# Kernel optimization log

Hardware: AMD Instinct MI355X
Metric: run time of the kernel (lower is better)

## Reference

```python
import jax, jax.numpy as jnp
import numpy as np

B, N, H = 4, 1024, 64

def setup_inputs() -> dict:
    key = jax.random.key(0)
    k1, k2, k3 = jax.random.split(key, 3)
    x = jax.random.normal(k1, (B, N, H), dtype=jnp.float32)
    # nn.Linear(2H, H): weight [H, 2H], bias [H]
    s1 = 1.0 / np.sqrt(2 * H)
    W1 = jax.random.uniform(k2, (H, 2 * H), minval=-s1, maxval=s1, dtype=jnp.float32)
    b1 = jnp.zeros((H,), dtype=jnp.float32)
    # nn.Linear(H, 1): weight [1, H], bias [1]
    s2 = 1.0 / np.sqrt(H)
    W2 = jax.random.uniform(k3, (1, H), minval=-s2, maxval=s2, dtype=jnp.float32)
    b2 = jnp.zeros((1,), dtype=jnp.float32)
    return {"x": x, "W1": W1, "b1": b1, "W2": W2, "b2": b2}

def reference(x, W1, b1, W2, b2):
    # cat([x_i, x_j]) @ W1.T == x_i @ W1a.T + x_j @ W1b.T  (decomposed; same math)
    W1a, W1b = W1[:, :x.shape[-1]], W1[:, x.shape[-1]:]
    hi = jnp.einsum('bid,hd->bih', x, W1a)            # [B,N,H]
    hj = jnp.einsum('bjd,hd->bjh', x, W1b)            # [B,N,H]
    h = jax.nn.relu(hi[:, :, None, :] + hj[:, None, :, :] + b1)  # [B,N,N,H]
    logits = jnp.einsum('bijh,h->bij', h, W2[0]) + b2[0]          # [B,N,N]
    attn = jax.nn.softmax(logits, axis=-1)
    updated = jnp.einsum('bij,bjd->bid', attn, x)     # [B,N,H]
    return updated, attn
```

## Files before the change

### kernel.cpp

```cpp
#include <hip/hip_runtime.h>

#define ATTN_OFF 262144

#define WS_HIP  0
#define WS_HJP  131072
#define WS_L16  262144
#define WS_SMAX 2359296
#define WS_SSUM 2424832
#define WS_PART 2490368

typedef float4 f4;
typedef _Float16 h2v __attribute__((ext_vector_type(2)));

union F4H { f4 f; h2v h[4]; };
union F2H { float2 f; h2v h[2]; };

__device__ __forceinline__ f4 ld4(const float* p) { return *reinterpret_cast<const f4*>(p); }
__device__ __forceinline__ void st4(float* p, f4 v) { *reinterpret_cast<f4*>(p) = v; }
__device__ __forceinline__ float fdot2f(h2v a, h2v b, float c) {
    return __builtin_amdgcn_fdot2(a, b, c, false);
}
__device__ __forceinline__ h2v pack2(float a, float b) {
    h2v r; r.x = (_Float16)a; r.y = (_Float16)b; return r;
}

__global__ __launch_bounds__(256, 4)
void ka_proj(const float* __restrict__ x, const float* __restrict__ W1,
             const float* __restrict__ b1,
             h2v* __restrict__ hiP, h2v* __restrict__ hjP) {
    __shared__ float xT[64 * 68];
    __shared__ float w1T[64 * 68];
    const int t  = threadIdx.x;
    const int i0 = blockIdx.x * 64;
    const int b  = blockIdx.y;
    const int z  = blockIdx.z;
    const int lo = t & 15;
    const int dq = t >> 4;
#pragma unroll
    for (int p = 0; p < 4; ++p) {
        const int il = p * 16 + lo;
        f4 v = ld4(&x[(size_t)(b * 1024 + i0 + il) * 64 + dq * 4]);
        xT[(dq * 4 + 0) * 68 + il] = v.x;
        xT[(dq * 4 + 1) * 68 + il] = v.y;
        xT[(dq * 4 + 2) * 68 + il] = v.z;
        xT[(dq * 4 + 3) * 68 + il] = v.w;
        f4 w = ld4(&W1[(size_t)il * 128 + z * 64 + dq * 4]);
        w1T[(dq * 4 + 0) * 68 + il] = w.x;
        w1T[(dq * 4 + 1) * 68 + il] = w.y;
        w1T[(dq * 4 + 2) * 68 + il] = w.z;
        w1T[(dq * 4 + 3) * 68 + il] = w.w;
    }
    __syncthreads();
    const int tx = t & 15;
    const int ty = t >> 4;
    float acc[4][4];
    if (z == 0) {
        f4 bv = ld4(&b1[tx * 4]);
        float ba[4] = {bv.x, bv.y, bv.z, bv.w};
#pragma unroll
        for (int ii = 0; ii < 4; ++ii)
#pragma unroll
            for (int cc = 0; cc < 4; ++cc) acc[ii][cc] = ba[cc];
    } else {
#pragma unroll
        for (int ii = 0; ii < 4; ++ii)
#pragma unroll
            for (int cc = 0; cc < 4; ++cc) acc[ii][cc] = 0.f;
    }
#pragma unroll 8
    for (int d = 0; d < 64; ++d) {
        f4 xv = ld4(&xT[d * 68 + ty * 4]);
        f4 wv = ld4(&w1T[d * 68 + tx * 4]);
        float xa[4] = {xv.x, xv.y, xv.z, xv.w};
        float wa[4] = {wv.x, wv.y, wv.z, wv.w};
#pragma unroll
        for (int ii = 0; ii < 4; ++ii)
#pragma unroll
            for (int cc = 0; cc < 4; ++cc)
                acc[ii][cc] = fmaf(xa[ii], wa[cc], acc[ii][cc]);
    }
    h2v* outp = z ? hjP : hiP;
#pragma unroll
    for (int p = 0; p < 2; ++p) {
        F4H u;
#pragma unroll
        for (int ii = 0; ii < 4; ++ii)
            u.h[ii] = pack2(acc[ii][p * 2 + 0], acc[ii][p * 2 + 1]);
        st4((float*)&outp[(size_t)(b * 32 + tx * 2 + p) * 1024 + i0 + ty * 4], u.f);
    }
}

__global__ __launch_bounds__(256, 4)
void kb_logits(const h2v* __restrict__ hiP, const h2v* __restrict__ hjP,
               const float* __restrict__ W2, _Float16* __restrict__ l16,
               float* __restrict__ smax, float* __restrict__ ssum) {
    __shared__ __align__(16) h2v s_hi[32 * 128];
    __shared__ __align__(16) h2v s_hj[32 * 64];
    __shared__ h2v s_w2[32];
    const int t  = threadIdx.x;
    const int jT = blockIdx.x;
    const int iT = blockIdx.y;
    const int b  = blockIdx.z;
#pragma unroll
    for (int p = 0; p < 4; ++p) {
        const int idx = p * 256 + t;
        const int hp  = idx >> 5;
        const int c4  = (idx & 31) * 4;
        st4((float*)&s_hi[hp * 128 + c4],
            ld4((const float*)&hiP[(size_t)(b * 32 + hp) * 1024 + iT * 128 + c4]));
    }
#pragma unroll
    for (int p = 0; p < 2; ++p) {
        const int idx = p * 256 + t;
        const int hp  = idx >> 4;
        const int c4  = (idx & 15) * 4;
        st4((float*)&s_hj[hp * 64 + c4],
            ld4((const float*)&hjP[(size_t)(b * 32 + hp) * 1024 + jT * 64 + c4]));
    }
    if (t < 16) {
        f4 w = ld4(&W2[t * 4]);
        s_w2[t * 2]     = pack2(w.x, w.y);
        s_w2[t * 2 + 1] = pack2(w.z, w.w);
    }
    __syncthreads();
    const int tx = t & 15;
    const int ty = t >> 4;
    float acc[8][4];
#pragma unroll
    for (int ii = 0; ii < 8; ++ii)
#pragma unroll
        for (int jj = 0; jj < 4; ++jj) acc[ii][jj] = 0.f;
    const h2v z2 = (h2v)0;
#pragma unroll 4
    for (int hp = 0; hp < 32; ++hp) {
        F4H a0, a1, bb;
        a0.f = ld4((const float*)&s_hi[hp * 128 + ty * 8]);
        a1.f = ld4((const float*)&s_hi[hp * 128 + ty * 8 + 4]);
        bb.f = ld4((const float*)&s_hj[hp * 64 + tx * 4]);
        const h2v w2p = s_w2[hp];
#pragma unroll
        for (int ii = 0; ii < 8; ++ii) {
            const h2v av = (ii < 4) ? a0.h[ii] : a1.h[ii - 4];
#pragma unroll
            for (int jj = 0; jj < 4; ++jj) {
                h2v r = __builtin_elementwise_max(av + bb.h[jj], z2);
                acc[ii][jj] = fdot2f(r, w2p, acc[ii][jj]);
            }
        }
    }
#pragma unroll
    for (int ii = 0; ii < 8; ++ii) {
        const int row = b * 1024 + iT * 128 + ty * 8 + ii;
        F2H uo;
        uo.h[0] = pack2(acc[ii][0], acc[ii][1]);
        uo.h[1] = pack2(acc[ii][2], acc[ii][3]);
        *reinterpret_cast<float2*>(&l16[(size_t)row * 1024 + jT * 64 + tx * 4]) = uo.f;
        float m = fmaxf(fmaxf(acc[ii][0], acc[ii][1]), fmaxf(acc[ii][2], acc[ii][3]));
#pragma unroll
        for (int d = 1; d < 16; d <<= 1) m = fmaxf(m, __shfl_xor(m, d));
        float s = __expf(acc[ii][0] - m) + __expf(acc[ii][1] - m) +
                  __expf(acc[ii][2] - m) + __expf(acc[ii][3] - m);
#pragma unroll
        for (int d = 1; d < 16; d <<= 1) s += __shfl_xor(s, d);
        if (tx == 0) {
            smax[jT * 4096 + row] = m;
            ssum[jT * 4096 + row] = s;
        }
    }
}

#define PS 132
__global__ __launch_bounds__(256, 2)
void kd_av(const _Float16* __restrict__ l16, const float* __restrict__ smax,
           const float* __restrict__ ssum, const float* __restrict__ x,
           float* __restrict__ attn, float* __restrict__ part) {
    __shared__ __align__(16) h2v s_p[32 * PS];
    __shared__ __align__(16) h2v s_x[32 * 64];
    __shared__ float s_m[128];
    __shared__ float s_il[128];
    const int t  = threadIdx.x;
    const int ks = blockIdx.x;
    const int iT = blockIdx.y;
    const int b  = blockIdx.z;
    const int j0 = ks * 64;
    const int gr = b * 1024 + iT * 128;
    if (t < 128) {
        float mv[16], sv[16];
#pragma unroll
        for (int c = 0; c < 16; ++c) {
            mv[c] = smax[c * 4096 + gr + t];
            sv[c] = ssum[c * 4096 + gr + t];
        }
        float M = mv[0];
#pragma unroll
        for (int c = 1; c < 16; ++c) M = fmaxf(M, mv[c]);
        float L = 0.f;
#pragma unroll
        for (int c = 0; c < 16; ++c) L += sv[c] * __expf(mv[c] - M);
        s_m[t]  = M;
        s_il[t] = 1.0f / L;
    }
#pragma unroll
    for (int it = 0; it < 2; ++it) {
        const int idx = it * 256 + t;
        const int jp  = idx >> 4;
        const int d4  = (idx & 15) * 4;
        f4 r0 = ld4(&x[(size_t)(b * 1024 + j0 + jp * 2)     * 64 + d4]);
        f4 r1 = ld4(&x[(size_t)(b * 1024 + j0 + jp * 2 + 1) * 64 + d4]);
        F4H u;
        u.h[0] = pack2(r0.x, r1.x); u.h[1] = pack2(r0.y, r1.y);
        u.h[2] = pack2(r0.z, r1.z); u.h[3] = pack2(r0.w, r1.w);
        st4((float*)&s_x[jp * 64 + d4], u.f);
    }
    __syncthreads();
#pragma unroll 2
    for (int it = 0; it < 4; ++it) {
        const int idx = it * 256 + t;
        const int rl  = idx >> 3;
        const int j8  = (idx & 7) * 8;
        F4H u;
        u.f = ld4((const float*)&l16[(size_t)(gr + rl) * 1024 + j0 + j8]);
        const float m  = s_m[rl];
        const float il = s_il[rl];
        float p[8];
#pragma unroll
        for (int k = 0; k < 4; ++k) {
            p[2 * k]     = __expf((float)u.h[k].x - m) * il;
            p[2 * k + 1] = __expf((float)u.h[k].y - m) * il;
        }
        float* ap = &attn[(size_t)(gr + rl) * 1024 + j0 + j8];
        st4(ap,     make_float4(p[0], p[1], p[2], p[3]));
        st4(ap + 4, make_float4(p[4], p[5], p[6], p[7]));
        const int jp0 = (idx & 7) * 4;
#pragma unroll
        for (int k = 0; k < 4; ++k)
            s_p[(jp0 + k) * PS + rl] = pack2(p[2 * k], p[2 * k + 1]);
    }
    __syncthreads();
    const int tx = t & 15;
    const int ty = t >> 4;
    float acc[8][4];
#pragma unroll
    for (int ii = 0; ii < 8; ++ii)
#pragma unroll
        for (int dd = 0; dd < 4; ++dd) acc[ii][dd] = 0.f;
#pragma unroll 4
    for (int jp = 0; jp < 32; ++jp) {
        F4H a0, a1, xv;
        a0.f = ld4((const float*)&s_p[jp * PS + ty * 8]);
        a1.f = ld4((const float*)&s_p[jp * PS + ty * 8 + 4]);
        xv.f = ld4((const float*)&s_x[jp * 64 + tx * 4]);
        h2v aa[8] = {a0.h[0], a0.h[1], a0.h[2], a0.h[3],
                     a1.h[0], a1.h[1], a1.h[2], a1.h[3]};
#pragma unroll
        for (int ii = 0; ii < 8; ++ii)
#pragma unroll
            for (int dd = 0; dd < 4; ++dd)
                acc[ii][dd] = fdot2f(aa[ii], xv.h[dd], acc[ii][dd]);
    }
#pragma unroll
    for (int ii = 0; ii < 8; ++ii) {
        f4 o = make_float4(acc[ii][0], acc[ii][1], acc[ii][2], acc[ii][3]);
        st4(&part[(size_t)(ks * 4096 + gr + ty * 8 + ii) * 64 + tx * 4], o);
    }
}

__global__ __launch_bounds__(256)
void ke_reduce(const float* __restrict__ part, float* __restrict__ out) {
    const int g = blockIdx.x * 256 + threadIdx.x;
    f4 a = ld4(&part[(size_t)g * 4]);
#pragma unroll
    for (int ks = 1; ks < 16; ++ks) {
        f4 v = ld4(&part[(size_t)ks * 262144 + g * 4]);
        a.x += v.x; a.y += v.y; a.z += v.z; a.w += v.w;
    }
    st4(&out[(size_t)g * 4], a);
}

extern "C" void kernel_launch(void* const* d_in, const int* in_sizes, int n_in,
                              void* d_out, int out_size, void* d_ws, size_t ws_size,
                              hipStream_t stream) {
    const float* x  = (const float*)d_in[0];
    const float* W1 = (const float*)d_in[1];
    const float* b1 = (const float*)d_in[2];
    const float* W2 = (const float*)d_in[3];
    float* out = (float*)d_out;
    float* ws  = (float*)d_ws;
    h2v*      hiP  = (h2v*)(ws + WS_HIP);
    h2v*      hjP  = (h2v*)(ws + WS_HJP);
    _Float16* l16  = (_Float16*)(ws + WS_L16);
    float*    smax = ws + WS_SMAX;
    float*    ssum = ws + WS_SSUM;
    float*    part = ws + WS_PART;

    ka_proj  <<<dim3(16, 4, 2), 256, 0, stream>>>(x, W1, b1, hiP, hjP);
    kb_logits<<<dim3(16, 8, 4), 256, 0, stream>>>(hiP, hjP, W2, l16, smax, ssum);
    kd_av    <<<dim3(16, 8, 4), 256, 0, stream>>>(l16, smax, ssum, x,
                                                  out + ATTN_OFF, part);
    ke_reduce<<<dim3(256),      256, 0, stream>>>(part, out);
}
```

Baseline: 105.2 us.

## Fuse logits, softmax and attention-value product into one row-block kernel

Replaces the three kernels for logits, softmax/AV and partial-sum reduction with one kernel. Each block owns 8 full query rows, so it computes the whole softmax in registers, writes attn once, and does the AV product with an in-LDS reduction. This removes the fp16 logits round trip, the separate max/sum statistics and the split-K partial buffer with its reduce launch. The cost is less parallelism per block, hj and x being re-read by every row block, and more LDS use. The projection kernel is also retiled to 32 rows per block to double its grid.

```diff
diff --git a/kernel.cpp b/kernel.cpp
--- a/kernel.cpp
+++ b/kernel.cpp
@@ -4,10 +4,6 @@
 
 #define WS_HIP  0
 #define WS_HJP  131072
-#define WS_L16  262144
-#define WS_SMAX 2359296
-#define WS_SSUM 2424832
-#define WS_PART 2490368
 
 typedef float4 f4;
 typedef _Float16 h2v __attribute__((ext_vector_type(2)));
@@ -28,253 +24,227 @@
 void ka_proj(const float* __restrict__ x, const float* __restrict__ W1,
              const float* __restrict__ b1,
              h2v* __restrict__ hiP, h2v* __restrict__ hjP) {
-    __shared__ float xT[64 * 68];
+    __shared__ float xT[64 * 36];
     __shared__ float w1T[64 * 68];
     const int t  = threadIdx.x;
-    const int i0 = blockIdx.x * 64;
+    const int i0 = blockIdx.x * 32;
     const int b  = blockIdx.y;
     const int z  = blockIdx.z;
     const int lo = t & 15;
     const int dq = t >> 4;
 #pragma unroll
-    for (int p = 0; p < 4; ++p) {
+    for (int p = 0; p < 2; ++p) {
         const int il = p * 16 + lo;
         f4 v = ld4(&x[(size_t)(b * 1024 + i0 + il) * 64 + dq * 4]);
-        xT[(dq * 4 + 0) * 68 + il] = v.x;
-        xT[(dq * 4 + 1) * 68 + il] = v.y;
-        xT[(dq * 4 + 2) * 68 + il] = v.z;
-        xT[(dq * 4 + 3) * 68 + il] = v.w;
-        f4 w = ld4(&W1[(size_t)il * 128 + z * 64 + dq * 4]);
-        w1T[(dq * 4 + 0) * 68 + il] = w.x;
-        w1T[(dq * 4 + 1) * 68 + il] = w.y;
-        w1T[(dq * 4 + 2) * 68 + il] = w.z;
-        w1T[(dq * 4 + 3) * 68 + il] = w.w;
+        xT[(dq * 4 + 0) * 36 + il] = v.x;
+        xT[(dq * 4 + 1) * 36 + il] = v.y;
+        xT[(dq * 4 + 2) * 36 + il] = v.z;
+        xT[(dq * 4 + 3) * 36 + il] = v.w;
+    }
+#pragma unroll
+    for (int p = 0; p < 4; ++p) {
+        const int cl = p * 16 + lo;
+        f4 w = ld4(&W1[(size_t)cl * 128 + z * 64 + dq * 4]);
+        w1T[(dq * 4 + 0) * 68 + cl] = w.x;
+        w1T[(dq * 4 + 1) * 68 + cl] = w.y;
+        w1T[(dq * 4 + 2) * 68 + cl] = w.z;
+        w1T[(dq * 4 + 3) * 68 + cl] = w.w;
     }
     __syncthreads();
     const int tx = t & 15;
     const int ty = t >> 4;
-    float acc[4][4];
+    float acc[2][4];
     if (z == 0) {
         f4 bv = ld4(&b1[tx * 4]);
-        float ba[4] = {bv.x, bv.y, bv.z, bv.w};
-#pragma unroll
-        for (int ii = 0; ii < 4; ++ii)
-#pragma unroll
-            for (int cc = 0; cc < 4; ++cc) acc[ii][cc] = ba[cc];
+        acc[0][0] = acc[1][0] = bv.x;
+        acc[0][1] = acc[1][1] = bv.y;
+        acc[0][2] = acc[1][2] = bv.z;
+        acc[0][3] = acc[1][3] = bv.w;
     } else {
 #pragma unroll
-        for (int ii = 0; ii < 4; ++ii)
+        for (int ii = 0; ii < 2; ++ii)
 #pragma unroll
             for (int cc = 0; cc < 4; ++cc) acc[ii][cc] = 0.f;
     }
 #pragma unroll 8
     for (int d = 0; d < 64; ++d) {
-        f4 xv = ld4(&xT[d * 68 + ty * 4]);
-        f4 wv = ld4(&w1T[d * 68 + tx * 4]);
-        float xa[4] = {xv.x, xv.y, xv.z, xv.w};
-        float wa[4] = {wv.x, wv.y, wv.z, wv.w};
-#pragma unroll
-        for (int ii = 0; ii < 4; ++ii)
-#pragma unroll
-            for (int cc = 0; cc < 4; ++cc)
-                acc[ii][cc] = fmaf(xa[ii], wa[cc], acc[ii][cc]);
+        const float2 xv = *reinterpret_cast<const float2*>(&xT[d * 36 + ty * 2]);
+        const f4 wv = ld4(&w1T[d * 68 + tx * 4]);
+        acc[0][0] = fmaf(xv.x, wv.x, acc[0][0]);
+        acc[0][1] = fmaf(xv.x, wv.y, acc[0][1]);
+        acc[0][2] = fmaf(xv.x, wv.z, acc[0][2]);
+        acc[0][3] = fmaf(xv.x, wv.w, acc[0][3]);
+        acc[1][0] = fmaf(xv.y, wv.x, acc[1][0]);
+        acc[1][1] = fmaf(xv.y, wv.y, acc[1][1]);
+        acc[1][2] = fmaf(xv.y, wv.z, acc[1][2]);
+        acc[1][3] = fmaf(xv.y, wv.w, acc[1][3]);
     }
     h2v* outp = z ? hjP : hiP;
 #pragma unroll
     for (int p = 0; p < 2; ++p) {
-        F4H u;
-#pragma unroll
-        for (int ii = 0; ii < 4; ++ii)
-            u.h[ii] = pack2(acc[ii][p * 2 + 0], acc[ii][p * 2 + 1]);
-        st4((float*)&outp[(size_t)(b * 32 + tx * 2 + p) * 1024 + i0 + ty * 4], u.f);
-    }
-}
-
-__global__ __launch_bounds__(256, 4)
-void kb_logits(const h2v* __restrict__ hiP, const h2v* __restrict__ hjP,
-               const float* __restrict__ W2, _Float16* __restrict__ l16,
-               float* __restrict__ smax, float* __restrict__ ssum) {
-    __shared__ __align__(16) h2v s_hi[32 * 128];
-    __shared__ __align__(16) h2v s_hj[32 * 64];
+        F2H uo;
+        uo.h[0] = pack2(acc[0][p * 2], acc[0][p * 2 + 1]);
+        uo.h[1] = pack2(acc[1][p * 2], acc[1][p * 2 + 1]);
+        *reinterpret_cast<float2*>(
+            &outp[(size_t)(b * 32 + tx * 2 + p) * 1024 + i0 + ty * 2]) = uo.f;
+    }
+}
+
+__global__ __launch_bounds__(256, 2)
+void kf_fused(const h2v* __restrict__ hiP, const h2v* __restrict__ hjP,
+              const float* __restrict__ W2, const float* __restrict__ x,
+              float* __restrict__ attn, float* __restrict__ upd) {
+    __shared__ union __align__(16) U {
+        h2v   hj[32 * 256];
+        h2v   xc[128 * 68];
+        float red[16 * 516];
+    } u;
+    __shared__ __align__(16) h2v s_p[512 * 12];
+    __shared__ h2v s_hi[32 * 8];
     __shared__ h2v s_w2[32];
+    __shared__ float s_il[8];
+
     const int t  = threadIdx.x;
-    const int jT = blockIdx.x;
-    const int iT = blockIdx.y;
-    const int b  = blockIdx.z;
-#pragma unroll
-    for (int p = 0; p < 4; ++p) {
-        const int idx = p * 256 + t;
-        const int hp  = idx >> 5;
-        const int c4  = (idx & 31) * 4;
-        st4((float*)&s_hi[hp * 128 + c4],
-            ld4((const float*)&hiP[(size_t)(b * 32 + hp) * 1024 + iT * 128 + c4]));
-    }
-#pragma unroll
-    for (int p = 0; p < 2; ++p) {
-        const int idx = p * 256 + t;
-        const int hp  = idx >> 4;
-        const int c4  = (idx & 15) * 4;
-        st4((float*)&s_hj[hp * 64 + c4],
-            ld4((const float*)&hjP[(size_t)(b * 32 + hp) * 1024 + jT * 64 + c4]));
+    const int i0 = blockIdx.x * 8;
+    const int b  = blockIdx.y;
+    const int tx = t & 31;
+    const int ty = t >> 5;
+    {
+        const int hp = t >> 3, ii8 = t & 7;
+        s_hi[hp * 8 + ii8] = hiP[(size_t)(b * 32 + hp) * 1024 + i0 + ii8];
     }
     if (t < 16) {
         f4 w = ld4(&W2[t * 4]);
         s_w2[t * 2]     = pack2(w.x, w.y);
         s_w2[t * 2 + 1] = pack2(w.z, w.w);
     }
+    float l[4][2][4];
+#pragma unroll
+    for (int c = 0; c < 4; ++c)
+#pragma unroll
+        for (int g = 0; g < 2; ++g)
+#pragma unroll
+            for (int k = 0; k < 4; ++k) l[c][g][k] = 0.f;
+    const h2v z2 = (h2v)0;
+#pragma unroll
+    for (int c = 0; c < 4; ++c) {
+#pragma unroll
+        for (int p = 0; p < 8; ++p) {
+            const int s = p * 256 + t;
+            const int hp = s >> 6, j4 = (s & 63) * 4;
+            st4((float*)&u.hj[hp * 256 + j4],
+                ld4((const float*)&hjP[(size_t)(b * 32 + hp) * 1024 + c * 256 + j4]));
+        }
+        __syncthreads();
+#pragma unroll 4
+        for (int hp = 0; hp < 32; ++hp) {
+            const h2v hv = s_hi[hp * 8 + ty];
+            const h2v wv = s_w2[hp];
+#pragma unroll
+            for (int g = 0; g < 2; ++g) {
+                F4H bb;
+                bb.f = ld4((const float*)&u.hj[hp * 256 + g * 128 + tx * 4]);
+#pragma unroll
+                for (int k = 0; k < 4; ++k) {
+                    h2v r = __builtin_elementwise_max(hv + bb.h[k], z2);
+                    l[c][g][k] = fdot2f(r, wv, l[c][g][k]);
+                }
+            }
+        }
+        __syncthreads();
+    }
+    float m = l[0][0][0];
+#pragma unroll
+    for (int c = 0; c < 4; ++c)
+#pragma unroll
+        for (int g = 0; g < 2; ++g)
+#pragma unroll
+            for (int k = 0; k < 4; ++k) m = fmaxf(m, l[c][g][k]);
+#pragma unroll
+    for (int d = 1; d < 32; d <<= 1) m = fmaxf(m, __shfl_xor(m, d));
+    float sum = 0.f;
+#pragma unroll
+    for (int c = 0; c < 4; ++c)
+#pragma unroll
+        for (int g = 0; g < 2; ++g)
+#pragma unroll
+            for (int k = 0; k < 4; ++k) {
+                l[c][g][k] = __expf(l[c][g][k] - m);
+                sum += l[c][g][k];
+            }
+#pragma unroll
+    for (int d = 1; d < 32; d <<= 1) sum += __shfl_xor(sum, d);
+    const float il = 1.0f / sum;
+    if (tx == 0) s_il[ty] = il;
+    const size_t arow = (size_t)(b * 1024 + i0 + ty) * 1024 + tx * 4;
+#pragma unroll
+    for (int c = 0; c < 4; ++c)
+#pragma unroll
+        for (int g = 0; g < 2; ++g) {
+            st4(&attn[arow + c * 256 + g * 128],
+                make_float4(l[c][g][0] * il, l[c][g][1] * il,
+                            l[c][g][2] * il, l[c][g][3] * il));
+            const int jp = c * 128 + g * 64 + tx * 2;
+            s_p[jp * 12 + ty]       = pack2(l[c][g][0], l[c][g][1]);
+            s_p[(jp + 1) * 12 + ty] = pack2(l[c][g][2], l[c][g][3]);
+        }
+    const int dq = t & 15, js = t >> 4;
+    float acc[8][4];
+#pragma unroll
+    for (int i = 0; i < 8; ++i)
+#pragma unroll
+        for (int q = 0; q < 4; ++q) acc[i][q] = 0.f;
+#pragma unroll
+    for (int c2 = 0; c2 < 4; ++c2) {
+        __syncthreads();
+#pragma unroll
+        for (int p = 0; p < 8; ++p) {
+            const int s = p * 256 + t;
+            const int jpl = s >> 4, dd = (s & 15) * 4;
+            const float* xr = &x[(size_t)(b * 1024 + c2 * 256 + jpl * 2) * 64 + dd];
+            f4 r0 = ld4(xr);
+            f4 r1 = ld4(xr + 64);
+            F4H pk;
+            pk.h[0] = pack2(r0.x, r1.x); pk.h[1] = pack2(r0.y, r1.y);
+            pk.h[2] = pack2(r0.z, r1.z); pk.h[3] = pack2(r0.w, r1.w);
+            st4((float*)&u.xc[jpl * 68 + dd], pk.f);
+        }
+        __syncthreads();
+#pragma unroll 2
+        for (int u8 = 0; u8 < 8; ++u8) {
+            const int jpl = u8 * 16 + js;
+            const int jp  = c2 * 128 + jpl;
+            F4H p0, p1, xv;
+            p0.f = ld4((const float*)&s_p[jp * 12]);
+            p1.f = ld4((const float*)&s_p[jp * 12 + 4]);
+            xv.f = ld4((const float*)&u.xc[jpl * 68 + dq * 4]);
+#pragma unroll
+            for (int i = 0; i < 8; ++i) {
+                const h2v pa = (i < 4) ? p0.h[i] : p1.h[i - 4];
+#pragma unroll
+                for (int q = 0; q < 4; ++q)
+                    acc[i][q] = fdot2f(pa, xv.h[q], acc[i][q]);
+            }
+        }
+    }
     __syncthreads();
-    const int tx = t & 15;
-    const int ty = t >> 4;
-    float acc[8][4];
-#pragma unroll
-    for (int ii = 0; ii < 8; ++ii)
-#pragma unroll
-        for (int jj = 0; jj < 4; ++jj) acc[ii][jj] = 0.f;
-    const h2v z2 = (h2v)0;
-#pragma unroll 4
-    for (int hp = 0; hp < 32; ++hp) {
-        F4H a0, a1, bb;
-        a0.f = ld4((const float*)&s_hi[hp * 128 + ty * 8]);
-        a1.f = ld4((const float*)&s_hi[hp * 128 + ty * 8 + 4]);
-        bb.f = ld4((const float*)&s_hj[hp * 64 + tx * 4]);
-        const h2v w2p = s_w2[hp];
-#pragma unroll
-        for (int ii = 0; ii < 8; ++ii) {
-            const h2v av = (ii < 4) ? a0.h[ii] : a1.h[ii - 4];
-#pragma unroll
-            for (int jj = 0; jj < 4; ++jj) {
-                h2v r = __builtin_elementwise_max(av + bb.h[jj], z2);
-                acc[ii][jj] = fdot2f(r, w2p, acc[ii][jj]);
-            }
-        }
-    }
-#pragma unroll
-    for (int ii = 0; ii < 8; ++ii) {
-        const int row = b * 1024 + iT * 128 + ty * 8 + ii;
-        F2H uo;
-        uo.h[0] = pack2(acc[ii][0], acc[ii][1]);
-        uo.h[1] = pack2(acc[ii][2], acc[ii][3]);
-        *reinterpret_cast<float2*>(&l16[(size_t)row * 1024 + jT * 64 + tx * 4]) = uo.f;
-        float m = fmaxf(fmaxf(acc[ii][0], acc[ii][1]), fmaxf(acc[ii][2], acc[ii][3]));
-#pragma unroll
-        for (int d = 1; d < 16; d <<= 1) m = fmaxf(m, __shfl_xor(m, d));
-        float s = __expf(acc[ii][0] - m) + __expf(acc[ii][1] - m) +
-                  __expf(acc[ii][2] - m) + __expf(acc[ii][3] - m);
-#pragma unroll
-        for (int d = 1; d < 16; d <<= 1) s += __shfl_xor(s, d);
-        if (tx == 0) {
-            smax[jT * 4096 + row] = m;
-            ssum[jT * 4096 + row] = s;
-        }
-    }
-}
-
-#define PS 132
-__global__ __launch_bounds__(256, 2)
-void kd_av(const _Float16* __restrict__ l16, const float* __restrict__ smax,
-           const float* __restrict__ ssum, const float* __restrict__ x,
-           float* __restrict__ attn, float* __restrict__ part) {
-    __shared__ __align__(16) h2v s_p[32 * PS];
-    __shared__ __align__(16) h2v s_x[32 * 64];
-    __shared__ float s_m[128];
-    __shared__ float s_il[128];
-    const int t  = threadIdx.x;
-    const int ks = blockIdx.x;
-    const int iT = blockIdx.y;
-    const int b  = blockIdx.z;
-    const int j0 = ks * 64;
-    const int gr = b * 1024 + iT * 128;
+#pragma unroll
+    for (int i = 0; i < 8; ++i)
+        st4(&u.red[js * 516 + i * 64 + dq * 4],
+            make_float4(acc[i][0], acc[i][1], acc[i][2], acc[i][3]));
+    __syncthreads();
     if (t < 128) {
-        float mv[16], sv[16];
-#pragma unroll
-        for (int c = 0; c < 16; ++c) {
-            mv[c] = smax[c * 4096 + gr + t];
-            sv[c] = ssum[c * 4096 + gr + t];
-        }
-        float M = mv[0];
-#pragma unroll
-        for (int c = 1; c < 16; ++c) M = fmaxf(M, mv[c]);
-        float L = 0.f;
-#pragma unroll
-        for (int c = 0; c < 16; ++c) L += sv[c] * __expf(mv[c] - M);
-        s_m[t]  = M;
-        s_il[t] = 1.0f / L;
-    }
-#pragma unroll
-    for (int it = 0; it < 2; ++it) {
-        const int idx = it * 256 + t;
-        const int jp  = idx >> 4;
-        const int d4  = (idx & 15) * 4;
-        f4 r0 = ld4(&x[(size_t)(b * 1024 + j0 + jp * 2)     * 64 + d4]);
-        f4 r1 = ld4(&x[(size_t)(b * 1024 + j0 + jp * 2 + 1) * 64 + d4]);
-        F4H u;
-        u.h[0] = pack2(r0.x, r1.x); u.h[1] = pack2(r0.y, r1.y);
-        u.h[2] = pack2(r0.z, r1.z); u.h[3] = pack2(r0.w, r1.w);
-        st4((float*)&s_x[jp * 64 + d4], u.f);
-    }
-    __syncthreads();
-#pragma unroll 2
-    for (int it = 0; it < 4; ++it) {
-        const int idx = it * 256 + t;
-        const int rl  = idx >> 3;
-        const int j8  = (idx & 7) * 8;
-        F4H u;
-        u.f = ld4((const float*)&l16[(size_t)(gr + rl) * 1024 + j0 + j8]);
-        const float m  = s_m[rl];
-        const float il = s_il[rl];
-        float p[8];
-#pragma unroll
-        for (int k = 0; k < 4; ++k) {
-            p[2 * k]     = __expf((float)u.h[k].x - m) * il;
-            p[2 * k + 1] = __expf((float)u.h[k].y - m) * il;
-        }
-        float* ap = &attn[(size_t)(gr + rl) * 1024 + j0 + j8];
-        st4(ap,     make_float4(p[0], p[1], p[2], p[3]));
-        st4(ap + 4, make_float4(p[4], p[5], p[6], p[7]));
-        const int jp0 = (idx & 7) * 4;
-#pragma unroll
-        for (int k = 0; k < 4; ++k)
-            s_p[(jp0 + k) * PS + rl] = pack2(p[2 * k], p[2 * k + 1]);
-    }
-    __syncthreads();
-    const int tx = t & 15;
-    const int ty = t >> 4;
-    float acc[8][4];
-#pragma unroll
-    for (int ii = 0; ii < 8; ++ii)
-#pragma unroll
-        for (int dd = 0; dd < 4; ++dd) acc[ii][dd] = 0.f;
-#pragma unroll 4
-    for (int jp = 0; jp < 32; ++jp) {
-        F4H a0, a1, xv;
-        a0.f = ld4((const float*)&s_p[jp * PS + ty * 8]);
-        a1.f = ld4((const float*)&s_p[jp * PS + ty * 8 + 4]);
-        xv.f = ld4((const float*)&s_x[jp * 64 + tx * 4]);
-        h2v aa[8] = {a0.h[0], a0.h[1], a0.h[2], a0.h[3],
-                     a1.h[0], a1.h[1], a1.h[2], a1.h[3]};
-#pragma unroll
-        for (int ii = 0; ii < 8; ++ii)
-#pragma unroll
-            for (int dd = 0; dd < 4; ++dd)
-                acc[ii][dd] = fdot2f(aa[ii], xv.h[dd], acc[ii][dd]);
-    }
-#pragma unroll
-    for (int ii = 0; ii < 8; ++ii) {
-        f4 o = make_float4(acc[ii][0], acc[ii][1], acc[ii][2], acc[ii][3]);
-        st4(&part[(size_t)(ks * 4096 + gr + ty * 8 + ii) * 64 + tx * 4], o);
-    }
-}
-
-__global__ __launch_bounds__(256)
-void ke_reduce(const float* __restrict__ part, float* __restrict__ out) {
-    const int g = blockIdx.x * 256 + threadIdx.x;
-    f4 a = ld4(&part[(size_t)g * 4]);
-#pragma unroll
-    for (int ks = 1; ks < 16; ++ks) {
-        f4 v = ld4(&part[(size_t)ks * 262144 + g * 4]);
-        a.x += v.x; a.y += v.y; a.z += v.z; a.w += v.w;
-    }
-    st4(&out[(size_t)g * 4], a);
+        const int i = t >> 4, dqq = t & 15;
+        f4 a = ld4(&u.red[i * 64 + dqq * 4]);
+#pragma unroll
+        for (int js2 = 1; js2 < 16; ++js2) {
+            f4 v = ld4(&u.red[js2 * 516 + i * 64 + dqq * 4]);
+            a.x += v.x; a.y += v.y; a.z += v.z; a.w += v.w;
+        }
+        const float sc = s_il[i];
+        st4(&upd[(size_t)(b * 1024 + i0 + i) * 64 + dqq * 4],
+            make_float4(a.x * sc, a.y * sc, a.z * sc, a.w * sc));
+    }
 }
 
 extern "C" void kernel_launch(void* const* d_in, const int* in_sizes, int n_in,
@@ -286,16 +256,9 @@
     const float* W2 = (const float*)d_in[3];
     float* out = (float*)d_out;
     float* ws  = (float*)d_ws;
-    h2v*      hiP  = (h2v*)(ws + WS_HIP);
-    h2v*      hjP  = (h2v*)(ws + WS_HJP);
-    _Float16* l16  = (_Float16*)(ws + WS_L16);
-    float*    smax = ws + WS_SMAX;
-    float*    ssum = ws + WS_SSUM;
-    float*    part = ws + WS_PART;
-
-    ka_proj  <<<dim3(16, 4, 2), 256, 0, stream>>>(x, W1, b1, hiP, hjP);
-    kb_logits<<<dim3(16, 8, 4), 256, 0, stream>>>(hiP, hjP, W2, l16, smax, ssum);
-    kd_av    <<<dim3(16, 8, 4), 256, 0, stream>>>(l16, smax, ssum, x,
-                                                  out + ATTN_OFF, part);
-    ke_reduce<<<dim3(256),      256, 0, stream>>>(part, out);
-}
+    h2v* hiP = (h2v*)(ws + WS_HIP);
+    h2v* hjP = (h2v*)(ws + WS_HJP);
+
+    ka_proj <<<dim3(32, 4, 2), 256, 0, stream>>>(x, W1, b1, hiP, hjP);
+    kf_fused<<<dim3(128, 4),   256, 0, stream>>>(hiP, hjP, W2, x, out + ATTN_OFF, out);
+}
```

After: 98.10 us. 6.8% less time.
